# Optimization experiments

Hardware: AMD Instinct MI355X
Metric: run time of the kernel (lower is better)

The kernel has to match this reference:

```python
import jax, jax.numpy as jnp
import numpy as np
from jax import lax

B, T, D = 8, 4096, 1024


def setup_inputs() -> dict:
    key = jax.random.key(0)
    ks = jax.random.split(key, 8)
    s = 1.0 / np.sqrt(D)  # keep GEMM outputs O(1)
    return {
        "x": jax.random.normal(ks[0], (B, T, D), dtype=jnp.float32),
        "state_p": jnp.zeros((B, D), dtype=jnp.float32),
        "decay": 0.8 + 0.19 * jax.random.uniform(ks[1], (D,), dtype=jnp.float32),  # ~0.9, stable
        "mass": jnp.ones((D,), dtype=jnp.float32),
        "Wq": s * jax.random.normal(ks[2], (D, D), dtype=jnp.float32),
        "bq": jnp.zeros((D,), dtype=jnp.float32),
        "Wk": s * jax.random.normal(ks[3], (D, D), dtype=jnp.float32),
        "bk": jnp.zeros((D,), dtype=jnp.float32),
        "Wv": s * jax.random.normal(ks[4], (D, D), dtype=jnp.float32),
        "bv": jnp.zeros((D,), dtype=jnp.float32),
    }


def reference(x, state_p, decay, mass, Wq, bq, Wk, bk, Wv, bv):
    # Batch all per-timestep projections into single GEMMs over (B*T) tokens.
    k_logit = jnp.einsum("btd,ed->bte", x, Wk) + bk        # [B,T,D]
    v = jnp.einsum("btd,ed->bte", x, Wv) + bv              # [B,T,D]
    u = jax.nn.sigmoid(k_logit) * v                          # gated input, [B,T,D]

    # Diagonal linear recurrence p_t = decay * p_{t-1} + u_t via scan over time.
    def step(p, u_t):
        p = p * decay + u_t
        return p, p

    final_p, ps = lax.scan(step, state_p, jnp.swapaxes(u, 0, 1))  # ps: [T,B,D]
    p = jnp.swapaxes(ps, 0, 1)                                     # [B,T,D]

    velocities = (jnp.einsum("btd,ed->bte", p, Wq) + bq) / mass    # [B,T,D]
    return velocities, final_p
```

## Files before the change

kernel.cpp:

```cpp
#include <hip/hip_runtime.h>
#include <stdint.h>
#include <stddef.h>

#define D_DIM 1024
#define T_LEN 4096
#define B_SZ 8
#define M_ROWS 32768
#define KTOT 1024
#define CHUNK 64
#define NCHUNK 64

typedef unsigned short u16;
typedef unsigned short u16x8 __attribute__((ext_vector_type(8)));
typedef __bf16 bf16x8 __attribute__((ext_vector_type(8)));
typedef float f32x4 __attribute__((ext_vector_type(4)));

__device__ __forceinline__ u16 f2bf(float f) {
    union { float f; unsigned u; } v; v.f = f;
    unsigned r = v.u + 0x7fffu + ((v.u >> 16) & 1u);
    return (u16)(r >> 16);
}
__device__ __forceinline__ float bf2f(u16 h) {
    union { unsigned u; float f; } v; v.u = ((unsigned)h) << 16;
    return v.f;
}

__global__ void convert_kernel(const float* __restrict__ src, u16* __restrict__ dst, int n4) {
    int i = blockIdx.x * blockDim.x + threadIdx.x;
    int stride = gridDim.x * blockDim.x;
    for (int j = i; j < n4; j += stride) {
        float4 v = ((const float4*)src)[j];
        ushort4 o;
        o.x = f2bf(v.x); o.y = f2bf(v.y); o.z = f2bf(v.z); o.w = f2bf(v.w);
        ((ushort4*)dst)[j] = o;
    }
}

__global__ void convert_w_kernel(const float* __restrict__ Wk, const float* __restrict__ Wv,
                                 const float* __restrict__ Wq,
                                 u16* __restrict__ wcat, u16* __restrict__ wqb) {
    int total = 3072 * 256;
    int stride = gridDim.x * blockDim.x;
    for (int idx = blockIdx.x * blockDim.x + threadIdx.x; idx < total; idx += stride) {
        int r = idx >> 8, c4 = idx & 255;
        const float* src; u16* dst;
        if (r < 2048) {
            int g = r >> 5, j = r & 31;
            src = (j < 16 ? Wk : Wv) + (size_t)(g * 16 + (j & 15)) * D_DIM;
            dst = wcat + (size_t)r * D_DIM;
        } else {
            src = Wq + (size_t)(r - 2048) * D_DIM;
            dst = wqb + (size_t)(r - 2048) * D_DIM;
        }
        float4 v = ((const float4*)src)[c4];
        ushort4 o;
        o.x = f2bf(v.x); o.y = f2bf(v.y); o.z = f2bf(v.z); o.w = f2bf(v.w);
        ((ushort4*)dst)[c4] = o;
    }
}

__device__ __forceinline__ void gload16(const u16* g, u16* l) {
    __builtin_amdgcn_global_load_lds(
        (const __attribute__((address_space(1))) void*)g,
        (__attribute__((address_space(3))) void*)l,
        16, 0, 0);
}

template<bool CAT>
__global__ __launch_bounds__(512, 2) void gemm9_kernel(
    const u16* __restrict__ A,
    const u16* __restrict__ Bg,
    const float* __restrict__ bias0,
    const float* __restrict__ bias1,
    u16* __restrict__ Uout,
    float* __restrict__ Fout)
{
    constexpr int NT = KTOT / 32;
    __shared__ u16 smem[4 * 16384];

    const int tid  = threadIdx.x;
    const int w    = tid >> 6;
    const int lane = tid & 63;

    const int cpx = gridDim.x >> 3;
    const int swz = (blockIdx.x & 7) * cpx + (blockIdx.x >> 3);
    const int nCol = CAT ? 8 : 4;
    const int M0 = (swz / nCol) * 256;
    const int N0 = (swz % nCol) * 256;

    const int srow = lane >> 2;
    const int sg   = (lane & 3) ^ ((srow >> 1) & 3);

    const u16* pA0 = A  + (size_t)(M0 + w * 32 +      srow) * KTOT + sg * 8;
    const u16* pA1 = A  + (size_t)(M0 + w * 32 + 16 + srow) * KTOT + sg * 8;
    const u16* pB0 = Bg + (size_t)(N0 + w * 32 +      srow) * KTOT + sg * 8;
    const u16* pB1 = Bg + (size_t)(N0 + w * 32 + 16 + srow) * KTOT + sg * 8;

    auto stage = [&](int buf) {
        u16* s = smem + buf * 16384;
        gload16(pA0, s + w * 1024);              pA0 += 32;
        gload16(pA1, s + w * 1024 + 512);        pA1 += 32;
        gload16(pB0, s + 8192 + w * 1024);       pB0 += 32;
        gload16(pB1, s + 8192 + w * 1024 + 512); pB1 += 32;
    };

    const int wrow = (w >> 2) * 128;
    const int wcol = (w & 3) * 64;
    const int fr = lane & 15;
    const int fq = lane >> 4;

    int offA[8], offB[4];
#pragma unroll
    for (int m = 0; m < 8; ++m) {
        int row = wrow + m * 16 + fr;
        offA[m] = row * 32 + ((fq ^ ((row >> 1) & 3)) << 3);
    }
#pragma unroll
    for (int n = 0; n < 4; ++n) {
        int row = wcol + n * 16 + fr;
        offB[n] = 8192 + row * 32 + ((fq ^ ((row >> 1) & 3)) << 3);
    }

    f32x4 acc[8][4] = {};
    bf16x8 aP[8], bP[4], aQ[8], bQ[4];

    stage(0); stage(1); stage(2);
    asm volatile("s_waitcnt vmcnt(8)" ::: "memory");
    __builtin_amdgcn_s_barrier();
#pragma unroll
    for (int m = 0; m < 8; ++m) aP[m] = *(const bf16x8*)(smem + offA[m]);
#pragma unroll
    for (int n = 0; n < 4; ++n) bP[n] = *(const bf16x8*)(smem + offB[n]);

#define SUBTILE(S, AC, BC, AN, BN_)                                                  \
  {                                                                                  \
    const int s_ = (S);                                                              \
    if (s_ + 1 < NT) {                                                               \
      if (s_ + 2 < NT) { asm volatile("s_waitcnt vmcnt(4)" ::: "memory"); }          \
      else             { asm volatile("s_waitcnt vmcnt(0)" ::: "memory"); }          \
    }                                                                                \
    __builtin_amdgcn_s_barrier();                                                    \
    asm volatile("s_waitcnt lgkmcnt(0)" ::: "memory");                               \
    __builtin_amdgcn_sched_barrier(0);                                               \
    if (s_ + 3 < NT) stage((s_ + 3) & 3);                                            \
    if (s_ + 1 < NT) {                                                               \
      const u16* nb_ = smem + ((s_ + 1) & 3) * 16384;                                \
      _Pragma("unroll") for (int m = 0; m < 8; ++m)                                  \
        AN[m] = *(const bf16x8*)(nb_ + offA[m]);                                     \
      _Pragma("unroll") for (int n = 0; n < 4; ++n)                                  \
        BN_[n] = *(const bf16x8*)(nb_ + offB[n]);                                    \
    }                                                                                \
    __builtin_amdgcn_s_setprio(1);                                                   \
    _Pragma("unroll") for (int m = 0; m < 8; ++m)                                    \
      _Pragma("unroll") for (int n = 0; n < 4; ++n)                                  \
        acc[m][n] = __builtin_amdgcn_mfma_f32_16x16x32_bf16(AC[m], BC[n], acc[m][n], 0, 0, 0); \
    __builtin_amdgcn_s_setprio(0);                                                   \
  }

#pragma unroll 1
    for (int s = 0; s < NT; s += 2) {
        SUBTILE(s,     aP, bP, aQ, bQ);
        SUBTILE(s + 1, aQ, bQ, aP, bP);
    }
#undef SUBTILE

    asm volatile("s_waitcnt lgkmcnt(0) vmcnt(0)" ::: "memory");

    if (CAT) {
        const int ucol0 = N0 / 2 + (w & 3) * 32;
#pragma unroll
        for (int p = 0; p < 2; ++p) {
            int col = ucol0 + p * 16 + fr;
            float b0 = bias0[col];
            float b1 = bias1[col];
#pragma unroll
            for (int m = 0; m < 8; ++m) {
                int row0 = M0 + wrow + m * 16 + fq * 4;
#pragma unroll
                for (int j = 0; j < 4; ++j) {
                    float kl = acc[m][2 * p][j] + b0;
                    float vv = acc[m][2 * p + 1][j] + b1;
                    float sig = 1.0f / (1.0f + __expf(-kl));
                    Uout[(size_t)(row0 + j) * D_DIM + col] = f2bf(sig * vv);
                }
            }
        }
    } else {
#pragma unroll
        for (int n = 0; n < 4; ++n) {
            int col = N0 + wcol + n * 16 + fr;
            float b0 = bias0[col];
            float b1 = bias1[col];
#pragma unroll
            for (int m = 0; m < 8; ++m) {
                int row0 = M0 + wrow + m * 16 + fq * 4;
#pragma unroll
                for (int j = 0; j < 4; ++j)
                    Fout[(size_t)(row0 + j) * D_DIM + col] = (acc[m][n][j] + b0) / b1;
            }
        }
    }
}

__global__ void chunk_carry_kernel(const u16* __restrict__ u, const float* __restrict__ decay,
                                   float* __restrict__ localc) {
    int id = blockIdx.x * blockDim.x + threadIdx.x;
    int d8 = id & 127;
    int c  = (id >> 7) & (NCHUNK - 1);
    int b  = id >> 13;
    float4 dlo = ((const float4*)decay)[d8 * 2];
    float4 dhi = ((const float4*)decay)[d8 * 2 + 1];
    float dec[8] = {dlo.x, dlo.y, dlo.z, dlo.w, dhi.x, dhi.y, dhi.z, dhi.w};
    float carry[8] = {};
    const u16* up = u + ((size_t)b * T_LEN + (size_t)c * CHUNK) * D_DIM + d8 * 8;
    for (int s = 0; s < CHUNK; ++s) {
        u16x8 v = *(const u16x8*)(up + (size_t)s * D_DIM);
#pragma unroll
        for (int j = 0; j < 8; ++j)
            carry[j] = fmaf(carry[j], dec[j], bf2f(v[j]));
    }
    float* lc = localc + ((size_t)(b * NCHUNK + c)) * D_DIM + d8 * 8;
#pragma unroll
    for (int j = 0; j < 8; ++j) lc[j] = carry[j];
}

__global__ void carry_scan_kernel(const float* __restrict__ localc, const float* __restrict__ state_p,
                                  const float* __restrict__ decay, float* __restrict__ prefix,
                                  float* __restrict__ final_p) {
    int id = blockIdx.x * blockDim.x + threadIdx.x;
    int d = id & (D_DIM - 1);
    int b = id >> 10;
    float dec = decay[d];
    float dl = dec;
#pragma unroll
    for (int i = 0; i < 6; ++i) dl *= dl;
    float P = state_p[id];
    for (int c = 0; c < NCHUNK; ++c) {
        int idx = (b * NCHUNK + c) * D_DIM + d;
        prefix[idx] = P;
        P = fmaf(P, dl, localc[idx]);
    }
    final_p[id] = P;
}

__global__ void reconstruct_kernel(u16* __restrict__ u, const float* __restrict__ decay,
                                   const float* __restrict__ prefix) {
    int id = blockIdx.x * blockDim.x + threadIdx.x;
    int d8 = id & 127;
    int c  = (id >> 7) & (NCHUNK - 1);
    int b  = id >> 13;
    float4 dlo = ((const float4*)decay)[d8 * 2];
    float4 dhi = ((const float4*)decay)[d8 * 2 + 1];
    float dec[8] = {dlo.x, dlo.y, dlo.z, dlo.w, dhi.x, dhi.y, dhi.z, dhi.w};
    const float* pf = prefix + ((size_t)(b * NCHUNK + c)) * D_DIM + d8 * 8;
    float p[8];
#pragma unroll
    for (int j = 0; j < 8; ++j) p[j] = pf[j];
    u16* up = u + ((size_t)b * T_LEN + (size_t)c * CHUNK) * D_DIM + d8 * 8;
    for (int s = 0; s < CHUNK; ++s) {
        u16x8 v = *(const u16x8*)(up + (size_t)s * D_DIM);
        u16x8 o;
#pragma unroll
        for (int j = 0; j < 8; ++j) {
            p[j] = fmaf(p[j], dec[j], bf2f(v[j]));
            o[j] = f2bf(p[j]);
        }
        *(u16x8*)(up + (size_t)s * D_DIM) = o;
    }
}

extern "C" void kernel_launch(void* const* d_in, const int* in_sizes, int n_in,
                              void* d_out, int out_size, void* d_ws, size_t ws_size,
                              hipStream_t stream) {
    const float* x       = (const float*)d_in[0];
    const float* state_p = (const float*)d_in[1];
    const float* decay   = (const float*)d_in[2];
    const float* mass    = (const float*)d_in[3];
    const float* Wq      = (const float*)d_in[4];
    const float* bq      = (const float*)d_in[5];
    const float* Wk      = (const float*)d_in[6];
    const float* bk      = (const float*)d_in[7];
    const float* Wv      = (const float*)d_in[8];
    const float* bv      = (const float*)d_in[9];

    float* out     = (float*)d_out;
    float* final_p = out + (size_t)M_ROWS * D_DIM;

    u16* xb = (u16*)d_out;

    u16* wcat = (u16*)d_ws;
    u16* wqb  = wcat + 2048 * 1024;
    u16* ub   = wqb + 1024 * 1024;
    float* localc = (float*)(ub + (size_t)M_ROWS * D_DIM);
    float* prefix = localc + B_SZ * NCHUNK * D_DIM;

    convert_kernel<<<4096, 256, 0, stream>>>(x, xb, (M_ROWS * D_DIM) / 4);
    convert_w_kernel<<<1536, 256, 0, stream>>>(Wk, Wv, Wq, wcat, wqb);

    gemm9_kernel<true><<<dim3(1024), dim3(512), 0, stream>>>(
        xb, wcat, bk, bv, ub, nullptr);

    chunk_carry_kernel<<<256, 256, 0, stream>>>(ub, decay, localc);
    carry_scan_kernel<<<32, 256, 0, stream>>>(localc, state_p, decay, prefix, final_p);
    reconstruct_kernel<<<256, 256, 0, stream>>>(ub, decay, prefix);

    gemm9_kernel<false><<<dim3(512), dim3(512), 0, stream>>>(
        ub, wqb, bq, mass, nullptr, out);
}
```

Measured before the change: 306.0 us.

## Load B operand fragments directly from global into registers, bypassing LDS

```diff
diff --git a/kernel.cpp b/kernel.cpp
--- a/kernel.cpp
+++ b/kernel.cpp
@@ -67,7 +67,7 @@
 }
 
 template<bool CAT>
-__global__ __launch_bounds__(512, 2) void gemm9_kernel(
+__global__ __launch_bounds__(512, 2) void gemm11_kernel(
     const u16* __restrict__ A,
     const u16* __restrict__ Bg,
     const float* __restrict__ bias0,
@@ -76,7 +76,7 @@
     float* __restrict__ Fout)
 {
     constexpr int NT = KTOT / 32;
-    __shared__ u16 smem[4 * 16384];
+    __shared__ u16 smem[4 * 8192];
 
     const int tid  = threadIdx.x;
     const int w    = tid >> 6;
@@ -91,17 +91,13 @@
     const int srow = lane >> 2;
     const int sg   = (lane & 3) ^ ((srow >> 1) & 3);
 
-    const u16* pA0 = A  + (size_t)(M0 + w * 32 +      srow) * KTOT + sg * 8;
-    const u16* pA1 = A  + (size_t)(M0 + w * 32 + 16 + srow) * KTOT + sg * 8;
-    const u16* pB0 = Bg + (size_t)(N0 + w * 32 +      srow) * KTOT + sg * 8;
-    const u16* pB1 = Bg + (size_t)(N0 + w * 32 + 16 + srow) * KTOT + sg * 8;
-
-    auto stage = [&](int buf) {
-        u16* s = smem + buf * 16384;
-        gload16(pA0, s + w * 1024);              pA0 += 32;
-        gload16(pA1, s + w * 1024 + 512);        pA1 += 32;
-        gload16(pB0, s + 8192 + w * 1024);       pB0 += 32;
-        gload16(pB1, s + 8192 + w * 1024 + 512); pB1 += 32;
+    const u16* pA0 = A + (size_t)(M0 + w * 32 +      srow) * KTOT + sg * 8;
+    const u16* pA1 = A + (size_t)(M0 + w * 32 + 16 + srow) * KTOT + sg * 8;
+
+    auto stageA = [&](int buf) {
+        u16* s = smem + buf * 8192;
+        gload16(pA0, s + w * 1024);       pA0 += 32;
+        gload16(pA1, s + w * 1024 + 512); pA1 += 32;
     };
 
     const int wrow = (w >> 2) * 128;
@@ -109,46 +105,43 @@
     const int fr = lane & 15;
     const int fq = lane >> 4;
 
-    int offA[8], offB[4];
+    int offA[8];
 #pragma unroll
     for (int m = 0; m < 8; ++m) {
         int row = wrow + m * 16 + fr;
         offA[m] = row * 32 + ((fq ^ ((row >> 1) & 3)) << 3);
     }
-#pragma unroll
-    for (int n = 0; n < 4; ++n) {
-        int row = wcol + n * 16 + fr;
-        offB[n] = 8192 + row * 32 + ((fq ^ ((row >> 1) & 3)) << 3);
-    }
+
+    const u16* pB[4];
+#pragma unroll
+    for (int n = 0; n < 4; ++n)
+        pB[n] = Bg + (size_t)(N0 + wcol + n * 16 + fr) * KTOT + fq * 8;
 
     f32x4 acc[8][4] = {};
-    bf16x8 aP[8], bP[4], aQ[8], bQ[4];
-
-    stage(0); stage(1); stage(2);
-    asm volatile("s_waitcnt vmcnt(8)" ::: "memory");
+    bf16x8 aP[8], aQ[8], bP[4], bQ[4];
+
+    stageA(0); stageA(1); stageA(2);
+#pragma unroll
+    for (int n = 0; n < 4; ++n) bP[n] = *(const bf16x8*)(pB[n]);
+    asm volatile("s_waitcnt vmcnt(4)" ::: "memory");
     __builtin_amdgcn_s_barrier();
 #pragma unroll
     for (int m = 0; m < 8; ++m) aP[m] = *(const bf16x8*)(smem + offA[m]);
-#pragma unroll
-    for (int n = 0; n < 4; ++n) bP[n] = *(const bf16x8*)(smem + offB[n]);
 
 #define SUBTILE(S, AC, BC, AN, BN_)                                                  \
   {                                                                                  \
     const int s_ = (S);                                                              \
-    if (s_ + 1 < NT) {                                                               \
-      if (s_ + 2 < NT) { asm volatile("s_waitcnt vmcnt(4)" ::: "memory"); }          \
-      else             { asm volatile("s_waitcnt vmcnt(0)" ::: "memory"); }          \
-    }                                                                                \
+    asm volatile("s_waitcnt vmcnt(6)" ::: "memory");                                 \
     __builtin_amdgcn_s_barrier();                                                    \
     asm volatile("s_waitcnt lgkmcnt(0)" ::: "memory");                               \
     __builtin_amdgcn_sched_barrier(0);                                               \
-    if (s_ + 3 < NT) stage((s_ + 3) & 3);                                            \
+    if (s_ + 3 < NT) stageA((s_ + 3) & 3);                                           \
     if (s_ + 1 < NT) {                                                               \
-      const u16* nb_ = smem + ((s_ + 1) & 3) * 16384;                                \
+      _Pragma("unroll") for (int n = 0; n < 4; ++n)                                  \
+        BN_[n] = *(const bf16x8*)(pB[n] + (size_t)(s_ + 1) * 32);                    \
+      const u16* nb_ = smem + ((s_ + 1) & 3) * 8192;                                 \
       _Pragma("unroll") for (int m = 0; m < 8; ++m)                                  \
         AN[m] = *(const bf16x8*)(nb_ + offA[m]);                                     \
-      _Pragma("unroll") for (int n = 0; n < 4; ++n)                                  \
-        BN_[n] = *(const bf16x8*)(nb_ + offB[n]);                                    \
     }                                                                                \
     __builtin_amdgcn_s_setprio(1);                                                   \
     _Pragma("unroll") for (int m = 0; m < 8; ++m)                                    \
@@ -297,13 +290,13 @@
     convert_kernel<<<4096, 256, 0, stream>>>(x, xb, (M_ROWS * D_DIM) / 4);
     convert_w_kernel<<<1536, 256, 0, stream>>>(Wk, Wv, Wq, wcat, wqb);
 
-    gemm9_kernel<true><<<dim3(1024), dim3(512), 0, stream>>>(
+    gemm11_kernel<true><<<dim3(1024), dim3(512), 0, stream>>>(
         xb, wcat, bk, bv, ub, nullptr);
 
     chunk_carry_kernel<<<256, 256, 0, stream>>>(ub, decay, localc);
     carry_scan_kernel<<<32, 256, 0, stream>>>(localc, state_p, decay, prefix, final_p);
     reconstruct_kernel<<<256, 256, 0, stream>>>(ub, decay, prefix);
 
-    gemm9_kernel<false><<<dim3(512), dim3(512), 0, stream>>>(
+    gemm11_kernel<false><<<dim3(512), dim3(512), 0, stream>>>(
         ub, wqb, bq, mass, nullptr, out);
 }
```

Measured after the change: 385.6 us. +26.0%, slower.
